# Kernel tuning notes

Hardware: AMD Instinct MI355X
Metric: run time of the kernel (lower is better)

## Reference

```python
import jax, jax.numpy as jnp
import numpy as np

B, C, H, W = 4, 256, 128, 128
K = 9  # 3x3 kernel taps


def _bilinear_gather(x, y, xq):
    """Bilinear sample x at float coords (y, xq) with zeros outside.
    x: [B,C,H,W]; y, xq: [B,K,H,W] -> returns [B,C,K,H,W]."""
    b, c, h, w = x.shape
    y0 = jnp.floor(y)
    x0 = jnp.floor(xq)
    wy = y - y0
    wx = xq - x0
    xf = x.reshape(b, c, h * w)

    def corner(yc, xc, wgt):
        valid = (yc >= 0) & (yc <= h - 1) & (xc >= 0) & (xc <= w - 1)
        yi = jnp.clip(yc, 0, h - 1).astype(jnp.int32)
        xi = jnp.clip(xc, 0, w - 1).astype(jnp.int32)
        idx = (yi * w + xi).reshape(b, -1)  # [B, K*H*W]
        g = jax.vmap(lambda xb, ib: jnp.take(xb, ib, axis=1))(xf, idx)
        g = g.reshape(b, c, *yc.shape[1:])  # [B,C,K,H,W]
        return g * (wgt * valid.astype(x.dtype))[:, None]

    v = corner(y0, x0, (1.0 - wy) * (1.0 - wx))
    v = v + corner(y0, x0 + 1.0, (1.0 - wy) * wx)
    v = v + corner(y0 + 1.0, x0, wy * (1.0 - wx))
    v = v + corner(y0 + 1.0, x0 + 1.0, wy * wx)
    return v


def setup_inputs() -> dict:
    key = jax.random.key(0)
    k1, k2, k3 = jax.random.split(key, 3)
    x = jax.random.normal(k1, (B, C, H, W), dtype=jnp.float32)
    offset = jax.random.normal(k2, (B, 2 * K, H, W), dtype=jnp.float32)
    weight = jax.random.normal(k3, (1, C, 3, 3), dtype=jnp.float32) / np.sqrt(C * K)
    bias = jnp.zeros((1,), dtype=jnp.float32)
    return {"x": x, "offset": offset, "weight": weight, "bias": bias}


def reference(x, offset, weight, bias):
    b, c, h, w = x.shape
    # offset channels ordered as (dy_k, dx_k) per kernel tap k (row-major 3x3)
    off = offset.reshape(b, K, 2, h, w)
    kyx = np.stack(np.meshgrid(np.arange(3), np.arange(3), indexing='ij'))  # [2,3,3]
    ky = jnp.asarray(kyx[0].reshape(K), x.dtype)
    kx = jnp.asarray(kyx[1].reshape(K), x.dtype)
    # sampling location: p0 (output pixel, stride 1, pad 1) + kernel tap + offset
    y = (jnp.arange(h, dtype=x.dtype)[None, None, :, None] - 1.0
         + ky[None, :, None, None] + off[:, :, 0])
    xq = (jnp.arange(w, dtype=x.dtype)[None, None, None, :] - 1.0
          + kx[None, :, None, None] + off[:, :, 1])
    sampled = _bilinear_gather(x, y, xq)  # [B,C,K,H,W]
    out = jnp.einsum('bckhw,ck->bhw', sampled, weight.reshape(c, K)) + bias
    return jax.nn.sigmoid(out)[:, None]  # [B,1,H,W]
```

## Files before the change

kernel.cpp:

```cpp
#include <hip/hip_runtime.h>
#include <math.h>

#define Bb 4
#define Cc 256
#define Hh 128
#define Ww 128
#define HW (Hh * Ww)
#define Kk 9

typedef float f32x4 __attribute__((ext_vector_type(4)));

__global__ __launch_bounds__(1024, 4) void proj_kernel(const float* __restrict__ x,
                                                       const float* __restrict__ w,
                                                       float* __restrict__ D) {
    const int tid   = threadIdx.x;
    const int lane  = tid & 63;
    const int wv    = tid >> 6;
    const int bid   = blockIdx.x;
    const int b     = bid >> 6;
    const int pbase = (bid & 63) << 8;
    const int p4    = pbase + lane * 4;

    const int cu = __builtin_amdgcn_readfirstlane(wv);
    const float* __restrict__ wp = w + cu * 16 * Kk;
    const float* __restrict__ xp = x + (size_t)(b * Cc + cu * 16) * HW + p4;

    f32x4 acc[Kk];
#pragma unroll
    for (int k = 0; k < Kk; ++k) acc[k] = (f32x4)(0.f);

#pragma unroll 4
    for (int ci = 0; ci < 16; ++ci) {
        const f32x4 xv = *reinterpret_cast<const f32x4*>(xp + (size_t)ci * HW);
#pragma unroll
        for (int k = 0; k < Kk; ++k) {
            const float wk = wp[ci * Kk + k];
            acc[k] = __builtin_elementwise_fma(xv, (f32x4)(wk), acc[k]);
        }
    }

    __shared__ f32x4 red[8][64][Kk];
    if (wv < 8) {
#pragma unroll
        for (int k = 0; k < Kk; ++k) red[wv][lane][k] = acc[k];
    }
    __syncthreads();
    if (wv >= 8) {
#pragma unroll
        for (int k = 0; k < Kk; ++k) red[wv - 8][lane][k] += acc[k];
    }
    __syncthreads();

    const float* __restrict__ redf = (const float*)red;
    for (int idx = tid; idx < 256 * Kk; idx += 1024) {
        const int k  = idx >> 8;
        const int px = idx & 255;
        const int base = (px >> 2) * (Kk * 4) + k * 4 + (px & 3);
        float s = 0.f;
#pragma unroll
        for (int g = 0; g < 8; ++g) s += redf[g * (64 * Kk * 4) + base];
        D[(b * Kk + k) * HW + pbase + px] = s;
    }
}

__global__ __launch_bounds__(512) void sample_kernel(const float* __restrict__ off,
                                                     const float* __restrict__ D,
                                                     const float* __restrict__ bias,
                                                     float* __restrict__ out) {
    const int tid   = threadIdx.x;
    const int px    = tid & 127;
    const int g     = tid >> 7;
    const int bid   = blockIdx.x;
    const int b     = bid >> 7;
    const int pbase = (bid & 127) << 7;
    const int p     = pbase + px;
    const int h     = p >> 7;
    const int w_    = p & (Ww - 1);

    const float* __restrict__ offb = off + (size_t)b * (2 * Kk) * HW + p;
    const float* __restrict__ Db   = D + (size_t)b * Kk * HW;

    float s = 0.f;

#define TAP(K)                                                                 \
    do {                                                                       \
        constexpr int kk = (K);                                                \
        constexpr int ky = kk / 3, kx = kk % 3;                                \
        const float dy = offb[(size_t)(2 * kk) * HW];                          \
        const float dx = offb[(size_t)(2 * kk + 1) * HW];                      \
        const float y  = (float)(h - 1 + ky) + dy;                             \
        const float xq = (float)(w_ - 1 + kx) + dx;                            \
        const float y0f = floorf(y);                                           \
        const float x0f = floorf(xq);                                          \
        const float wy  = y - y0f;                                             \
        const float wx  = xq - x0f;                                            \
        const int y0 = (int)y0f;                                               \
        const int x0 = (int)x0f;                                               \
        const float* __restrict__ Dk = Db + kk * HW;                           \
        {                                                                      \
            const int yy = y0, xx = x0;                                        \
            const bool valid = (yy >= 0) & (yy < Hh) & (xx >= 0) & (xx < Ww);  \
            const int yi = min(max(yy, 0), Hh - 1);                            \
            const int xi = min(max(xx, 0), Ww - 1);                            \
            const float v = Dk[yi * Ww + xi];                                  \
            s += valid ? (1.f - wy) * (1.f - wx) * v : 0.f;                    \
        }                                                                      \
        {                                                                      \
            const int yy = y0, xx = x0 + 1;                                    \
            const bool valid = (yy >= 0) & (yy < Hh) & (xx >= 0) & (xx < Ww);  \
            const int yi = min(max(yy, 0), Hh - 1);                            \
            const int xi = min(max(xx, 0), Ww - 1);                            \
            const float v = Dk[yi * Ww + xi];                                  \
            s += valid ? (1.f - wy) * wx * v : 0.f;                            \
        }                                                                      \
        {                                                                      \
            const int yy = y0 + 1, xx = x0;                                    \
            const bool valid = (yy >= 0) & (yy < Hh) & (xx >= 0) & (xx < Ww);  \
            const int yi = min(max(yy, 0), Hh - 1);                            \
            const int xi = min(max(xx, 0), Ww - 1);                            \
            const float v = Dk[yi * Ww + xi];                                  \
            s += valid ? wy * (1.f - wx) * v : 0.f;                            \
        }                                                                      \
        {                                                                      \
            const int yy = y0 + 1, xx = x0 + 1;                                \
            const bool valid = (yy >= 0) & (yy < Hh) & (xx >= 0) & (xx < Ww);  \
            const int yi = min(max(yy, 0), Hh - 1);                            \
            const int xi = min(max(xx, 0), Ww - 1);                            \
            const float v = Dk[yi * Ww + xi];                                  \
            s += valid ? wy * wx * v : 0.f;                                    \
        }                                                                      \
    } while (0)

    if (g == 0) {
        TAP(0); TAP(4); TAP(8);
    } else if (g == 1) {
        TAP(1); TAP(5);
    } else if (g == 2) {
        TAP(2); TAP(6);
    } else {
        TAP(3); TAP(7);
    }
#undef TAP

    __shared__ float part[4][128];
    part[g][px] = s;
    __syncthreads();

    if (tid < 128) {
        const float t = part[0][px] + part[1][px] + part[2][px] + part[3][px] + bias[0];
        out[(b << 14) + pbase + px] = 1.f / (1.f + expf(-t));
    }
}

extern "C" void kernel_launch(void* const* d_in, const int* in_sizes, int n_in,
                              void* d_out, int out_size, void* d_ws, size_t ws_size,
                              hipStream_t stream) {
    const float* x    = (const float*)d_in[0];
    const float* off  = (const float*)d_in[1];
    const float* w    = (const float*)d_in[2];
    const float* bias = (const float*)d_in[3];
    float* out        = (float*)d_out;

    float* D = (float*)d_ws;

    proj_kernel<<<256, 1024, 0, stream>>>(x, w, D);
    sample_kernel<<<512, 512, 0, stream>>>(off, D, bias, out);
}
```

Before: 103.1 us.

## Split channel reduction across blocks with partial planes and a combine kernel

The projection kernel now splits the channel dimension into four groups across blocks. Each block handles 1024 pixels over 64 channels with 512 threads, reduces two halves in shared memory, and writes a partial D plane. A new combine kernel sums the four partial planes before sampling. This cuts the per-block shared-memory reduction and gives each thread a longer channel loop, at the cost of extra global traffic (four partial planes written and read back) and one more kernel launch.

```diff
diff --git a/kernel.cpp b/kernel.cpp
--- a/kernel.cpp
+++ b/kernel.cpp
@@ -7,60 +7,64 @@
 #define Ww 128
 #define HW (Hh * Ww)
 #define Kk 9
+#define PLANE (Bb * Kk * HW)
 
 typedef float f32x4 __attribute__((ext_vector_type(4)));
 
-__global__ __launch_bounds__(1024, 4) void proj_kernel(const float* __restrict__ x,
-                                                       const float* __restrict__ w,
-                                                       float* __restrict__ D) {
-    const int tid   = threadIdx.x;
-    const int lane  = tid & 63;
-    const int wv    = tid >> 6;
-    const int bid   = blockIdx.x;
-    const int b     = bid >> 6;
-    const int pbase = (bid & 63) << 8;
-    const int p4    = pbase + lane * 4;
+__global__ __launch_bounds__(512) void proj_kernel(const float* __restrict__ x,
+                                                   const float* __restrict__ w,
+                                                   float* __restrict__ Dp) {
+    const int tid  = threadIdx.x;
+    const int pxq  = tid & 255;
+    const int half = tid >> 8;
+    const int bid  = blockIdx.x;
+    const int b    = bid >> 6;
+    const int cg   = (bid >> 4) & 3;
+    const int tile = bid & 15;
+    const int pb   = tile << 10;
 
-    const int cu = __builtin_amdgcn_readfirstlane(wv);
-    const float* __restrict__ wp = w + cu * 16 * Kk;
-    const float* __restrict__ xp = x + (size_t)(b * Cc + cu * 16) * HW + p4;
+    const int c0 = cg * 64 + __builtin_amdgcn_readfirstlane(half);
+    const float* __restrict__ wp = w + c0 * Kk;
+    const float* __restrict__ xp = x + (size_t)(b * Cc + c0) * HW + pb + pxq * 4;
 
     f32x4 acc[Kk];
 #pragma unroll
     for (int k = 0; k < Kk; ++k) acc[k] = (f32x4)(0.f);
 
-#pragma unroll 4
-    for (int ci = 0; ci < 16; ++ci) {
-        const f32x4 xv = *reinterpret_cast<const f32x4*>(xp + (size_t)ci * HW);
+#pragma unroll 8
+    for (int ci = 0; ci < 32; ++ci) {
+        const f32x4 xv = *reinterpret_cast<const f32x4*>(xp + (size_t)(2 * ci) * HW);
 #pragma unroll
         for (int k = 0; k < Kk; ++k) {
-            const float wk = wp[ci * Kk + k];
+            const float wk = wp[ci * 2 * Kk + k];
             acc[k] = __builtin_elementwise_fma(xv, (f32x4)(wk), acc[k]);
         }
     }
 
-    __shared__ f32x4 red[8][64][Kk];
-    if (wv < 8) {
+    __shared__ f32x4 red[256][Kk];
+    if (half == 1) {
 #pragma unroll
-        for (int k = 0; k < Kk; ++k) red[wv][lane][k] = acc[k];
+        for (int k = 0; k < Kk; ++k) red[pxq][k] = acc[k];
     }
     __syncthreads();
-    if (wv >= 8) {
+    if (half == 0) {
+        float* __restrict__ dst = Dp + (size_t)cg * PLANE;
 #pragma unroll
-        for (int k = 0; k < Kk; ++k) red[wv - 8][lane][k] += acc[k];
+        for (int k = 0; k < Kk; ++k) {
+            const f32x4 v = acc[k] + red[pxq][k];
+            *reinterpret_cast<f32x4*>(dst + (size_t)(b * Kk + k) * HW + pb + pxq * 4) = v;
+        }
     }
-    __syncthreads();
+}
 
-    const float* __restrict__ redf = (const float*)red;
-    for (int idx = tid; idx < 256 * Kk; idx += 1024) {
-        const int k  = idx >> 8;
-        const int px = idx & 255;
-        const int base = (px >> 2) * (Kk * 4) + k * 4 + (px & 3);
-        float s = 0.f;
-#pragma unroll
-        for (int g = 0; g < 8; ++g) s += redf[g * (64 * Kk * 4) + base];
-        D[(b * Kk + k) * HW + pbase + px] = s;
-    }
+__global__ __launch_bounds__(256) void combine_kernel(const float* __restrict__ Dp,
+                                                      float* __restrict__ Dsum) {
+    const int i = (blockIdx.x * 256 + threadIdx.x) * 4;
+    const f32x4 a = *reinterpret_cast<const f32x4*>(Dp + 0 * (size_t)PLANE + i);
+    const f32x4 b = *reinterpret_cast<const f32x4*>(Dp + 1 * (size_t)PLANE + i);
+    const f32x4 c = *reinterpret_cast<const f32x4*>(Dp + 2 * (size_t)PLANE + i);
+    const f32x4 d = *reinterpret_cast<const f32x4*>(Dp + 3 * (size_t)PLANE + i);
+    *reinterpret_cast<f32x4*>(Dsum + i) = (a + b) + (c + d);
 }
 
 __global__ __launch_bounds__(512) void sample_kernel(const float* __restrict__ off,
@@ -161,8 +165,10 @@
     const float* bias = (const float*)d_in[3];
     float* out        = (float*)d_out;
 
-    float* D = (float*)d_ws;
+    float* Dp   = (float*)d_ws;
+    float* Dsum = Dp + 4 * (size_t)PLANE;
 
-    proj_kernel<<<256, 1024, 0, stream>>>(x, w, D);
-    sample_kernel<<<512, 512, 0, stream>>>(off, D, bias, out);
+    proj_kernel<<<256, 512, 0, stream>>>(x, w, Dp);
+    combine_kernel<<<PLANE / 1024, 256, 0, stream>>>(Dp, Dsum);
+    sample_kernel<<<512, 512, 0, stream>>>(off, Dsum, bias, out);
 }
```

Result: slower. 110.9 us (+7.5%).

## Fuse projection and sampling kernels into one cooperative launch with grid sync

Applied to the files above, without the earlier changes.

Merges the channel-projection kernel and the bilinear sampling kernel into a single cooperative kernel that separates the two phases with a grid-wide barrier. The sampling phase now runs on 256 blocks of 1024 threads and reuses the reduction shared memory for its partial sums. The aim is to drop the second kernel launch and the inter-kernel gap. In exchange it adds grid sync overhead, requires all 256 blocks to be co-resident, and the sampling phase runs with fewer blocks than before.

```diff
diff --git a/kernel.cpp b/kernel.cpp
--- a/kernel.cpp
+++ b/kernel.cpp
@@ -1,5 +1,8 @@
 #include <hip/hip_runtime.h>
+#include <hip/hip_cooperative_groups.h>
 #include <math.h>
+
+namespace cg = cooperative_groups;
 
 #define Bb 4
 #define Cc 256
@@ -10,77 +13,77 @@
 
 typedef float f32x4 __attribute__((ext_vector_type(4)));
 
-__global__ __launch_bounds__(1024, 4) void proj_kernel(const float* __restrict__ x,
-                                                       const float* __restrict__ w,
-                                                       float* __restrict__ D) {
+__global__ __launch_bounds__(1024, 4) void fused_kernel(const float* __restrict__ x,
+                                                        const float* __restrict__ w,
+                                                        const float* __restrict__ off,
+                                                        const float* __restrict__ bias,
+                                                        float* __restrict__ D,
+                                                        float* __restrict__ out) {
     const int tid   = threadIdx.x;
     const int lane  = tid & 63;
     const int wv    = tid >> 6;
     const int bid   = blockIdx.x;
     const int b     = bid >> 6;
     const int pbase = (bid & 63) << 8;
-    const int p4    = pbase + lane * 4;
 
-    const int cu = __builtin_amdgcn_readfirstlane(wv);
-    const float* __restrict__ wp = w + cu * 16 * Kk;
-    const float* __restrict__ xp = x + (size_t)(b * Cc + cu * 16) * HW + p4;
+    __shared__ f32x4 red[8][64][Kk];
 
-    f32x4 acc[Kk];
+    {
+        const int p4 = pbase + lane * 4;
+        const int cu = __builtin_amdgcn_readfirstlane(wv);
+        const float* __restrict__ wp = w + cu * 16 * Kk;
+        const float* __restrict__ xp = x + (size_t)(b * Cc + cu * 16) * HW + p4;
+
+        f32x4 acc[Kk];
 #pragma unroll
-    for (int k = 0; k < Kk; ++k) acc[k] = (f32x4)(0.f);
+        for (int k = 0; k < Kk; ++k) acc[k] = (f32x4)(0.f);
 
 #pragma unroll 4
-    for (int ci = 0; ci < 16; ++ci) {
-        const f32x4 xv = *reinterpret_cast<const f32x4*>(xp + (size_t)ci * HW);
+        for (int ci = 0; ci < 16; ++ci) {
+            const f32x4 xv = *reinterpret_cast<const f32x4*>(xp + (size_t)ci * HW);
 #pragma unroll
-        for (int k = 0; k < Kk; ++k) {
-            const float wk = wp[ci * Kk + k];
-            acc[k] = __builtin_elementwise_fma(xv, (f32x4)(wk), acc[k]);
+            for (int k = 0; k < Kk; ++k) {
+                const float wk = wp[ci * Kk + k];
+                acc[k] = __builtin_elementwise_fma(xv, (f32x4)(wk), acc[k]);
+            }
+        }
+
+        if (wv < 8) {
+#pragma unroll
+            for (int k = 0; k < Kk; ++k) red[wv][lane][k] = acc[k];
+        }
+        __syncthreads();
+        if (wv >= 8) {
+#pragma unroll
+            for (int k = 0; k < Kk; ++k) red[wv - 8][lane][k] += acc[k];
+        }
+        __syncthreads();
+
+        const float* __restrict__ redf = (const float*)red;
+        for (int idx = tid; idx < 256 * Kk; idx += 1024) {
+            const int k  = idx >> 8;
+            const int px = idx & 255;
+            const int base = (px >> 2) * (Kk * 4) + k * 4 + (px & 3);
+            float s = 0.f;
+#pragma unroll
+            for (int g = 0; g < 8; ++g) s += redf[g * (64 * Kk * 4) + base];
+            D[(b * Kk + k) * HW + pbase + px] = s;
         }
     }
 
-    __shared__ f32x4 red[8][64][Kk];
-    if (wv < 8) {
-#pragma unroll
-        for (int k = 0; k < Kk; ++k) red[wv][lane][k] = acc[k];
-    }
-    __syncthreads();
-    if (wv >= 8) {
-#pragma unroll
-        for (int k = 0; k < Kk; ++k) red[wv - 8][lane][k] += acc[k];
-    }
-    __syncthreads();
+    cg::this_grid().sync();
 
-    const float* __restrict__ redf = (const float*)red;
-    for (int idx = tid; idx < 256 * Kk; idx += 1024) {
-        const int k  = idx >> 8;
-        const int px = idx & 255;
-        const int base = (px >> 2) * (Kk * 4) + k * 4 + (px & 3);
+    {
+        const int px = tid & 255;
+        const int g  = tid >> 8;
+        const int p  = pbase + px;
+        const int h  = p >> 7;
+        const int w_ = p & (Ww - 1);
+
+        const float* __restrict__ offb = off + (size_t)b * (2 * Kk) * HW + p;
+        const float* __restrict__ Db   = D + (size_t)b * Kk * HW;
+
         float s = 0.f;
-#pragma unroll
-        for (int g = 0; g < 8; ++g) s += redf[g * (64 * Kk * 4) + base];
-        D[(b * Kk + k) * HW + pbase + px] = s;
-    }
-}
-
-__global__ __launch_bounds__(512) void sample_kernel(const float* __restrict__ off,
-                                                     const float* __restrict__ D,
-                                                     const float* __restrict__ bias,
-                                                     float* __restrict__ out) {
-    const int tid   = threadIdx.x;
-    const int px    = tid & 127;
-    const int g     = tid >> 7;
-    const int bid   = blockIdx.x;
-    const int b     = bid >> 7;
-    const int pbase = (bid & 127) << 7;
-    const int p     = pbase + px;
-    const int h     = p >> 7;
-    const int w_    = p & (Ww - 1);
-
-    const float* __restrict__ offb = off + (size_t)b * (2 * Kk) * HW + p;
-    const float* __restrict__ Db   = D + (size_t)b * Kk * HW;
-
-    float s = 0.f;
 
 #define TAP(K)                                                                 \
     do {                                                                       \
@@ -131,24 +134,26 @@
         }                                                                      \
     } while (0)
 
-    if (g == 0) {
-        TAP(0); TAP(4); TAP(8);
-    } else if (g == 1) {
-        TAP(1); TAP(5);
-    } else if (g == 2) {
-        TAP(2); TAP(6);
-    } else {
-        TAP(3); TAP(7);
-    }
+        if (g == 0) {
+            TAP(0); TAP(4); TAP(8);
+        } else if (g == 1) {
+            TAP(1); TAP(5);
+        } else if (g == 2) {
+            TAP(2); TAP(6);
+        } else {
+            TAP(3); TAP(7);
+        }
 #undef TAP
 
-    __shared__ float part[4][128];
-    part[g][px] = s;
-    __syncthreads();
+        float* __restrict__ part = (float*)red;
+        part[g * 256 + px] = s;
+        __syncthreads();
 
-    if (tid < 128) {
-        const float t = part[0][px] + part[1][px] + part[2][px] + part[3][px] + bias[0];
-        out[(b << 14) + pbase + px] = 1.f / (1.f + expf(-t));
+        if (tid < 256) {
+            const float t = part[tid] + part[256 + tid] + part[512 + tid] +
+                            part[768 + tid] + bias[0];
+            out[(b << 14) + pbase + tid] = 1.f / (1.f + expf(-t));
+        }
     }
 }
 
@@ -163,6 +168,8 @@
 
     float* D = (float*)d_ws;
 
-    proj_kernel<<<256, 1024, 0, stream>>>(x, w, D);
-    sample_kernel<<<512, 512, 0, stream>>>(off, D, bias, out);
+    void* args[] = {(void*)&x, (void*)&w, (void*)&off, (void*)&bias,
+                    (void*)&D, (void*)&out};
+    hipLaunchCooperativeKernel((const void*)fused_kernel, dim3(256), dim3(1024),
+                               args, 0, stream);
 }
```

New measurement: 146.7 us. 42.3% more time.
